# Kernel optimization log

Measured on AMD Instinct MI355X. Metric: run time of the kernel, lower is better.

The kernel has to match this reference:

```python
import jax, jax.numpy as jnp
import numpy as np

N_NODES = 100000
N_EDGES = 1600000
D_IN = 64
D_H = 64
D_LIN = 256
D_OUT = 128
N_GRAPHS = 64
BN_EPS = 1e-5


def setup_inputs() -> dict:
    key = jax.random.key(0)
    ks = jax.random.split(key, 16)

    def lin(k, fan_in, fan_out):
        # kaiming-ish init, scale 1/sqrt(fan_in)
        return jax.random.normal(k, (fan_in, fan_out), jnp.float32) / np.float32(np.sqrt(fan_in))

    inp = {}
    inp["x"] = jax.random.normal(ks[0], (N_NODES, D_IN), jnp.float32)
    inp["edge_index"] = jax.random.randint(ks[1], (2, N_EDGES), 0, N_NODES, jnp.int32)
    inp["batch"] = jnp.sort(jax.random.randint(ks[2], (N_NODES,), 0, N_GRAPHS, jnp.int32))

    dims = [(D_IN, D_H), (D_H, D_H), (D_H, D_H)]
    ki = 3
    for l, (di, do) in enumerate(dims):
        inp[f"conv{l}_w1"] = lin(ks[ki], di, do); ki += 1
        inp[f"conv{l}_b1"] = jnp.zeros((do,), jnp.float32)
        inp[f"conv{l}_w2"] = lin(ks[ki], do, do); ki += 1
        inp[f"conv{l}_b2"] = jnp.zeros((do,), jnp.float32)
    for l in range(2):
        inp[f"bn{l}_gamma"] = jnp.ones((D_H,), jnp.float32)
        inp[f"bn{l}_beta"] = jnp.zeros((D_H,), jnp.float32)
    inp["mp_w1"] = lin(ks[ki], D_H, D_LIN); ki += 1
    inp["mp_b1"] = jnp.zeros((D_LIN,), jnp.float32)
    inp["mp_w2"] = lin(ks[ki], D_LIN, D_OUT)
    inp["mp_b2"] = jnp.zeros((D_OUT,), jnp.float32)
    return inp


def gin_conv(x, src, dst, w1, b1, w2, b2):
    # GINConv with eps=0: nn((1+eps)*x + sum_{j->i} x_j)
    agg = jax.ops.segment_sum(x[src], dst, num_segments=N_NODES)  # [N, d]
    h = x + agg
    h = jnp.maximum(h @ w1 + b1, 0.0)
    return h @ w2 + b2


def batch_norm(x, gamma, beta):
    # BatchNorm1d over node dim (training-mode batch statistics)
    mean = jnp.mean(x, axis=0)
    var = jnp.var(x, axis=0)
    return (x - mean) * jax.lax.rsqrt(var + BN_EPS) * gamma + beta


def reference(x, edge_index, batch,
              conv0_w1, conv0_b1, conv0_w2, conv0_b2,
              conv1_w1, conv1_b1, conv1_w2, conv1_b2,
              conv2_w1, conv2_b1, conv2_w2, conv2_b2,
              bn0_gamma, bn0_beta, bn1_gamma, bn1_beta,
              mp_w1, mp_b1, mp_w2, mp_b2):
    src, dst = edge_index[0], edge_index[1]
    convs = [(conv0_w1, conv0_b1, conv0_w2, conv0_b2),
             (conv1_w1, conv1_b1, conv1_w2, conv1_b2),
             (conv2_w1, conv2_b1, conv2_w2, conv2_b2)]
    bns = [(bn0_gamma, bn0_beta), (bn1_gamma, bn1_beta)]

    h = x
    # first conv_num_layers-1 layers: conv -> BN -> ReLU (dropout = identity in eval)
    for i in range(2):
        w1, b1, w2, b2 = convs[i]
        h = gin_conv(h, src, dst, w1, b1, w2, b2)
        h = batch_norm(h, bns[i][0], bns[i][1])
        h = jnp.maximum(h, 0.0)
    # last conv
    w1, b1, w2, b2 = convs[2]
    h = gin_conv(h, src, dst, w1, b1, w2, b2)
    # global add pool over graphs
    pooled = jax.ops.segment_sum(h, batch, num_segments=N_GRAPHS)  # [G, d]
    emb = pooled
    out = jnp.maximum(pooled @ mp_w1 + mp_b1, 0.0)  # dropout = identity in eval
    out = out @ mp_w2 + mp_b2
    return (out, emb)
```

## Files before the change

kernel.cpp:

```cpp
#include <hip/hip_runtime.h>

#define N_NODES 100000
#define N_EDGES 1600000
#define D 64
#define N_GRAPHS 64
#define D_LIN 256
#define D_OUT 128
#define BN_EPS 1e-5f

typedef unsigned short ushort;
typedef unsigned int uint;

__device__ __forceinline__ float4 ld4(const float* p) { return *(const float4*)p; }

__device__ __forceinline__ uint f2bf(float f) {
  uint u = __float_as_uint(f);
  return (u + 0x7FFFu + ((u >> 16) & 1u)) >> 16;
}

__global__ __launch_bounds__(256) void k_cvt(const float* __restrict__ in,
                                             ushort* __restrict__ out, int n8) {
  int i = blockIdx.x * 256 + threadIdx.x;
  if (i < n8) {
    float4 a = ((const float4*)in)[2 * i];
    float4 b = ((const float4*)in)[2 * i + 1];
    uint4 o;
    o.x = f2bf(a.x) | (f2bf(a.y) << 16);
    o.y = f2bf(a.z) | (f2bf(a.w) << 16);
    o.z = f2bf(b.x) | (f2bf(b.y) << 16);
    o.w = f2bf(b.z) | (f2bf(b.w) << 16);
    ((uint4*)out)[i] = o;
  }
}

__global__ void k_count(const int* __restrict__ dstA, int* __restrict__ deg) {
  int i = blockIdx.x * blockDim.x + threadIdx.x;
  if (i < N_EDGES) atomicAdd(&deg[dstA[i]], 1);
}

__global__ void k_blocksum(const int* __restrict__ deg, int* __restrict__ bsum) {
  __shared__ int s[256];
  int t = threadIdx.x, i = blockIdx.x * 256 + t;
  s[t] = (i < N_NODES) ? deg[i] : 0;
  __syncthreads();
  for (int off = 128; off > 0; off >>= 1) {
    if (t < off) s[t] += s[t + off];
    __syncthreads();
  }
  if (t == 0) bsum[blockIdx.x] = s[0];
}

__global__ void k_scanblocks(const int* __restrict__ bsum, int* __restrict__ boff, int nb) {
  __shared__ int s[512];
  int t = threadIdx.x;
  int v = (t < nb) ? bsum[t] : 0;
  s[t] = v;
  __syncthreads();
  for (int off = 1; off < 512; off <<= 1) {
    int u = (t >= off) ? s[t - off] : 0;
    __syncthreads();
    s[t] += u;
    __syncthreads();
  }
  if (t < nb) boff[t] = s[t] - v;
}

__global__ void k_scanfinal(const int* __restrict__ deg, const int* __restrict__ boff,
                            int* __restrict__ rowptr, int* __restrict__ rowcur) {
  __shared__ int s[256];
  int t = threadIdx.x, i = blockIdx.x * 256 + t;
  int d = (i < N_NODES) ? deg[i] : 0;
  s[t] = d;
  __syncthreads();
  for (int off = 1; off < 256; off <<= 1) {
    int u = (t >= off) ? s[t - off] : 0;
    __syncthreads();
    s[t] += u;
    __syncthreads();
  }
  if (i < N_NODES) {
    int v = boff[blockIdx.x] + s[t] - d;
    rowptr[i] = v;
    rowcur[i] = v;
  }
  if (i == 0) rowptr[N_NODES] = N_EDGES;
}

__global__ void k_fill(const int* __restrict__ srcA, const int* __restrict__ dstA,
                       int* __restrict__ rowcur, int* __restrict__ colidx) {
  int i = blockIdx.x * blockDim.x + threadIdx.x;
  if (i < N_EDGES) {
    int d = dstA[i];
    int pos = atomicAdd(&rowcur[d], 1);
    colidx[pos] = srcA[i];
  }
}

template <int APPLY_BN, int EMIT_STATS, int OUT_BF>
__global__ __launch_bounds__(256, 6) void k_conv(
    const ushort* __restrict__ h_in, const float* __restrict__ ss,
    const int* __restrict__ rowptr, const int* __restrict__ colidx,
    const float* __restrict__ w1, const float* __restrict__ b1,
    const float* __restrict__ w2, const float* __restrict__ b2,
    float* __restrict__ h_out_f, ushort* __restrict__ h_out_bf,
    float* __restrict__ stats) {
  __shared__ float sT[64][68];
  __shared__ float sSum[64], sSq[64];

  const int tid = threadIdx.x;
  const int wave = tid >> 6, lane = tid & 63;
  const int eg = lane >> 3;
  const int fl = (lane & 7) << 3;
  const int row0 = blockIdx.x * 64;

  if (EMIT_STATS && tid < 64) { sSum[tid] = 0.f; sSq[tid] = 0.f; }

  float sc[8], sh[8];
  if (APPLY_BN) {
    float4 a = ld4(&ss[fl]), b = ld4(&ss[fl + 4]);
    float4 c = ld4(&ss[64 + fl]), d = ld4(&ss[64 + fl + 4]);
    sc[0] = a.x; sc[1] = a.y; sc[2] = a.z; sc[3] = a.w;
    sc[4] = b.x; sc[5] = b.y; sc[6] = b.z; sc[7] = b.w;
    sh[0] = c.x; sh[1] = c.y; sh[2] = c.z; sh[3] = c.w;
    sh[4] = d.x; sh[5] = d.y; sh[6] = d.z; sh[7] = d.w;
  }

#define ACC8(u)                                                        \
  {                                                                    \
    float f0 = __uint_as_float((u).x << 16);                           \
    float f1 = __uint_as_float((u).x & 0xffff0000u);                   \
    float f2 = __uint_as_float((u).y << 16);                           \
    float f3 = __uint_as_float((u).y & 0xffff0000u);                   \
    float f4 = __uint_as_float((u).z << 16);                           \
    float f5 = __uint_as_float((u).z & 0xffff0000u);                   \
    float f6 = __uint_as_float((u).w << 16);                           \
    float f7 = __uint_as_float((u).w & 0xffff0000u);                   \
    if (APPLY_BN) {                                                    \
      f0 = fmaxf(fmaf(f0, sc[0], sh[0]), 0.f);                         \
      f1 = fmaxf(fmaf(f1, sc[1], sh[1]), 0.f);                         \
      f2 = fmaxf(fmaf(f2, sc[2], sh[2]), 0.f);                         \
      f3 = fmaxf(fmaf(f3, sc[3], sh[3]), 0.f);                         \
      f4 = fmaxf(fmaf(f4, sc[4], sh[4]), 0.f);                         \
      f5 = fmaxf(fmaf(f5, sc[5], sh[5]), 0.f);                         \
      f6 = fmaxf(fmaf(f6, sc[6], sh[6]), 0.f);                         \
      f7 = fmaxf(fmaf(f7, sc[7], sh[7]), 0.f);                         \
    }                                                                  \
    acc[0] += f0; acc[1] += f1; acc[2] += f2; acc[3] += f3;            \
    acc[4] += f4; acc[5] += f5; acc[6] += f6; acc[7] += f7;            \
  }

  for (int rr = 0; rr < 16; ++rr) {
    const int r = (wave << 4) + rr;
    const int row = row0 + r;
    float acc[8] = {0.f, 0.f, 0.f, 0.f, 0.f, 0.f, 0.f, 0.f};
    if (row < N_NODES) {
      if (eg == 0) {
        uint4 u = *(const uint4*)(h_in + ((size_t)row << 6) + fl);
        ACC8(u);
      }
      const int e0 = rowptr[row], e1 = rowptr[row + 1];
      int e = e0 + eg;
      for (; e + 8 < e1; e += 16) {
        int s0 = colidx[e];
        int s1 = colidx[e + 8];
        uint4 u0 = *(const uint4*)(h_in + ((size_t)s0 << 6) + fl);
        uint4 u1 = *(const uint4*)(h_in + ((size_t)s1 << 6) + fl);
        ACC8(u0);
        ACC8(u1);
      }
      if (e < e1) {
        int s0 = colidx[e];
        uint4 u0 = *(const uint4*)(h_in + ((size_t)s0 << 6) + fl);
        ACC8(u0);
      }
#pragma unroll
      for (int j = 0; j < 8; ++j) {
        acc[j] += __shfl_xor(acc[j], 8);
        acc[j] += __shfl_xor(acc[j], 16);
        acc[j] += __shfl_xor(acc[j], 32);
      }
    }
    if (lane < 8) {
      *(float4*)&sT[r][fl] = make_float4(acc[0], acc[1], acc[2], acc[3]);
      *(float4*)&sT[r][fl + 4] = make_float4(acc[4], acc[5], acc[6], acc[7]);
    }
  }
#undef ACC8
  __syncthreads();

  const int tc = tid & 15, tr = tid >> 4;

  float hreg[4][4];
  {
    float acc[4][4];
#pragma unroll
    for (int i = 0; i < 4; ++i)
#pragma unroll
      for (int j = 0; j < 4; ++j) acc[i][j] = 0.f;
#pragma unroll 8
    for (int k = 0; k < 64; ++k) {
      const float4 b = ld4(&w1[(k << 6) + (tc << 2)]);
#pragma unroll
      for (int i = 0; i < 4; ++i) {
        const float a = sT[(tr << 2) + i][k];
        acc[i][0] = fmaf(a, b.x, acc[i][0]);
        acc[i][1] = fmaf(a, b.y, acc[i][1]);
        acc[i][2] = fmaf(a, b.z, acc[i][2]);
        acc[i][3] = fmaf(a, b.w, acc[i][3]);
      }
    }
    const float4 bb = ld4(&b1[tc << 2]);
#pragma unroll
    for (int i = 0; i < 4; ++i) {
      hreg[i][0] = fmaxf(acc[i][0] + bb.x, 0.f);
      hreg[i][1] = fmaxf(acc[i][1] + bb.y, 0.f);
      hreg[i][2] = fmaxf(acc[i][2] + bb.z, 0.f);
      hreg[i][3] = fmaxf(acc[i][3] + bb.w, 0.f);
    }
  }
  __syncthreads();
#pragma unroll
  for (int i = 0; i < 4; ++i)
    *(float4*)&sT[(tr << 2) + i][tc << 2] = *(float4*)&hreg[i][0];
  __syncthreads();

  {
    float acc[4][4];
#pragma unroll
    for (int i = 0; i < 4; ++i)
#pragma unroll
      for (int j = 0; j < 4; ++j) acc[i][j] = 0.f;
#pragma unroll 8
    for (int k = 0; k < 64; ++k) {
      const float4 b = ld4(&w2[(k << 6) + (tc << 2)]);
#pragma unroll
      for (int i = 0; i < 4; ++i) {
        const float a = sT[(tr << 2) + i][k];
        acc[i][0] = fmaf(a, b.x, acc[i][0]);
        acc[i][1] = fmaf(a, b.y, acc[i][1]);
        acc[i][2] = fmaf(a, b.z, acc[i][2]);
        acc[i][3] = fmaf(a, b.w, acc[i][3]);
      }
    }
    const float4 bb = ld4(&b2[tc << 2]);
    float p[4] = {0.f, 0.f, 0.f, 0.f}, q[4] = {0.f, 0.f, 0.f, 0.f};
#pragma unroll
    for (int i = 0; i < 4; ++i) {
      const int row = row0 + (tr << 2) + i;
      float4 o;
      o.x = acc[i][0] + bb.x;
      o.y = acc[i][1] + bb.y;
      o.z = acc[i][2] + bb.z;
      o.w = acc[i][3] + bb.w;
      if (row < N_NODES) {
        if (OUT_BF) {
          uint2 o2;
          o2.x = f2bf(o.x) | (f2bf(o.y) << 16);
          o2.y = f2bf(o.z) | (f2bf(o.w) << 16);
          *(uint2*)(h_out_bf + ((size_t)row << 6) + (tc << 2)) = o2;
        } else {
          *(float4*)&h_out_f[row * 64 + (tc << 2)] = o;
        }
        if (EMIT_STATS) {
          p[0] += o.x; q[0] += o.x * o.x;
          p[1] += o.y; q[1] += o.y * o.y;
          p[2] += o.z; q[2] += o.z * o.z;
          p[3] += o.w; q[3] += o.w * o.w;
        }
      }
    }
    if (EMIT_STATS) {
#pragma unroll
      for (int j = 0; j < 4; ++j) {
        atomicAdd(&sSum[(tc << 2) + j], p[j]);
        atomicAdd(&sSq[(tc << 2) + j], q[j]);
      }
      __syncthreads();
      if (tid < 64) {
        atomicAdd(&stats[tid], sSum[tid]);
        atomicAdd(&stats[64 + tid], sSq[tid]);
      }
    }
  }
}

__global__ void k_bnfin(const float* __restrict__ stats, const float* __restrict__ gamma,
                        const float* __restrict__ beta, float* __restrict__ ss) {
  int t = threadIdx.x;
  if (t < 64) {
    const float inv_n = 1.f / (float)N_NODES;
    float mean = stats[t] * inv_n;
    float var = stats[64 + t] * inv_n - mean * mean;
    float scale = gamma[t] * rsqrtf(var + BN_EPS);
    ss[t] = scale;
    ss[64 + t] = beta[t] - mean * scale;
  }
}

__global__ __launch_bounds__(256) void k_pool(const float* __restrict__ h,
                                              const int* __restrict__ batch,
                                              float* __restrict__ emb) {
  const int NW = 1024;
  const int RPW = (N_NODES + NW - 1) / NW;
  int wid = (blockIdx.x * 256 + threadIdx.x) >> 6;
  int lane = threadIdx.x & 63;
  int r0 = wid * RPW;
  if (r0 >= N_NODES) return;
  int r1 = min(r0 + RPW, N_NODES);
  float acc = 0.f;
  int curg = batch[r0];
  for (int i = r0; i < r1; ++i) {
    int g = batch[i];
    if (g != curg) {
      atomicAdd(&emb[curg * 64 + lane], acc);
      acc = 0.f;
      curg = g;
    }
    acc += h[i * 64 + lane];
  }
  atomicAdd(&emb[curg * 64 + lane], acc);
}

__global__ __launch_bounds__(256) void k_mlp(const float* __restrict__ emb,
                                             const float* __restrict__ w1,
                                             const float* __restrict__ b1,
                                             const float* __restrict__ w2,
                                             const float* __restrict__ b2,
                                             float* __restrict__ out) {
  __shared__ float sp[64];
  __shared__ float smid[256];
  int g = blockIdx.x, t = threadIdx.x;
  if (t < 64) sp[t] = emb[g * 64 + t];
  __syncthreads();
  float acc = b1[t];
#pragma unroll 8
  for (int k = 0; k < 64; ++k) acc = fmaf(sp[k], w1[k * 256 + t], acc);
  smid[t] = fmaxf(acc, 0.f);
  __syncthreads();
  if (t < 128) {
    float o = b2[t];
#pragma unroll 8
    for (int k = 0; k < 256; ++k) o = fmaf(smid[k], w2[k * 128 + t], o);
    out[g * 128 + t] = o;
  }
}

extern "C" void kernel_launch(void* const* d_in, const int* in_sizes, int n_in,
                              void* d_out, int out_size, void* d_ws, size_t ws_size,
                              hipStream_t stream) {
  const float* x = (const float*)d_in[0];
  const int* edge = (const int*)d_in[1];
  const int* batch = (const int*)d_in[2];
  const float* cw1[3] = {(const float*)d_in[3], (const float*)d_in[7], (const float*)d_in[11]};
  const float* cb1[3] = {(const float*)d_in[4], (const float*)d_in[8], (const float*)d_in[12]};
  const float* cw2[3] = {(const float*)d_in[5], (const float*)d_in[9], (const float*)d_in[13]};
  const float* cb2[3] = {(const float*)d_in[6], (const float*)d_in[10], (const float*)d_in[14]};
  const float* bng[2] = {(const float*)d_in[15], (const float*)d_in[17]};
  const float* bnb[2] = {(const float*)d_in[16], (const float*)d_in[18]};
  const float* mpw1 = (const float*)d_in[19];
  const float* mpb1 = (const float*)d_in[20];
  const float* mpw2 = (const float*)d_in[21];
  const float* mpb2 = (const float*)d_in[22];

  char* ws = (char*)d_ws;
  size_t off = 0;
  auto alloc = [&](size_t bytes) {
    void* p = ws + off;
    off = (off + bytes + 255) & ~(size_t)255;
    return p;
  };
  int* rowptr = (int*)alloc((N_NODES + 1) * sizeof(int));
  int* rowcur = (int*)alloc(N_NODES * sizeof(int));
  int* colidx = (int*)alloc(N_EDGES * sizeof(int));
  int* bsum = (int*)alloc(512 * sizeof(int));
  int* boff = (int*)alloc(512 * sizeof(int));
  ushort* x_bf = (ushort*)alloc((size_t)N_NODES * 64 * sizeof(ushort));
  ushort* hA_bf = (ushort*)alloc((size_t)N_NODES * 64 * sizeof(ushort));
  ushort* hB_bf = (ushort*)alloc((size_t)N_NODES * 64 * sizeof(ushort));
  float* stats = (float*)alloc(2 * 128 * sizeof(float));
  float* ssbuf = (float*)alloc(2 * 128 * sizeof(float));
  float* hF = (float*)x_bf;

  float* outp = (float*)d_out;
  float* emb = outp + N_GRAPHS * D_OUT;

  const int* srcA = edge;
  const int* dstA = edge + N_EDGES;

  hipMemsetAsync(rowcur, 0, N_NODES * sizeof(int), stream);
  hipMemsetAsync(stats, 0, 2 * 128 * sizeof(float), stream);
  hipMemsetAsync(emb, 0, N_GRAPHS * 64 * sizeof(float), stream);

  const int NB = (N_NODES + 255) / 256;
  const int EB = (N_EDGES + 255) / 256;
  k_cvt<<<(N_NODES * 64 / 8 + 255) / 256, 256, 0, stream>>>(x, x_bf, N_NODES * 64 / 8);
  k_count<<<EB, 256, 0, stream>>>(dstA, rowcur);
  k_blocksum<<<NB, 256, 0, stream>>>(rowcur, bsum);
  k_scanblocks<<<1, 512, 0, stream>>>(bsum, boff, NB);
  k_scanfinal<<<NB, 256, 0, stream>>>(rowcur, boff, rowptr, rowcur);
  k_fill<<<EB, 256, 0, stream>>>(srcA, dstA, rowcur, colidx);

  const int GC = (N_NODES + 63) / 64;
  k_conv<0, 1, 1><<<GC, 256, 0, stream>>>(x_bf, nullptr, rowptr, colidx, cw1[0], cb1[0],
                                          cw2[0], cb2[0], nullptr, hA_bf, stats);
  k_bnfin<<<1, 64, 0, stream>>>(stats, bng[0], bnb[0], ssbuf);
  k_conv<1, 1, 1><<<GC, 256, 0, stream>>>(hA_bf, ssbuf, rowptr, colidx, cw1[1], cb1[1],
                                          cw2[1], cb2[1], nullptr, hB_bf, stats + 128);
  k_bnfin<<<1, 64, 0, stream>>>(stats + 128, bng[1], bnb[1], ssbuf + 128);
  k_conv<1, 0, 0><<<GC, 256, 0, stream>>>(hB_bf, ssbuf + 128, rowptr, colidx, cw1[2],
                                          cb1[2], cw2[2], cb2[2], hF, nullptr, nullptr);

  k_pool<<<256, 256, 0, stream>>>(hF, batch, emb);
  k_mlp<<<N_GRAPHS, 256, 0, stream>>>(emb, mpw1, mpb1, mpw2, mpb2, outp);
}
```

Before: 537.9 us.

## Build CSR via bucketed two-pass binning and shrink conv blocks to 32 rows

Result: no change. 534.0 us (-0.7%).

```diff
diff --git a/kernel.cpp b/kernel.cpp
--- a/kernel.cpp
+++ b/kernel.cpp
@@ -7,6 +7,8 @@
 #define D_LIN 256
 #define D_OUT 128
 #define BN_EPS 1e-5f
+#define NBUCK 782
+#define BIN_CH 16384
 
 typedef unsigned short ushort;
 typedef unsigned int uint;
@@ -33,85 +35,132 @@
   }
 }
 
-__global__ void k_count(const int* __restrict__ dstA, int* __restrict__ deg) {
-  int i = blockIdx.x * blockDim.x + threadIdx.x;
-  if (i < N_EDGES) atomicAdd(&deg[dstA[i]], 1);
-}
-
-__global__ void k_blocksum(const int* __restrict__ deg, int* __restrict__ bsum) {
-  __shared__ int s[256];
-  int t = threadIdx.x, i = blockIdx.x * 256 + t;
-  s[t] = (i < N_NODES) ? deg[i] : 0;
-  __syncthreads();
-  for (int off = 128; off > 0; off >>= 1) {
-    if (t < off) s[t] += s[t + off];
-    __syncthreads();
-  }
-  if (t == 0) bsum[blockIdx.x] = s[0];
-}
-
-__global__ void k_scanblocks(const int* __restrict__ bsum, int* __restrict__ boff, int nb) {
-  __shared__ int s[512];
+
+__global__ __launch_bounds__(256) void k_hist(const int* __restrict__ dstA,
+                                              int* __restrict__ bcnt) {
+  __shared__ int lh[NBUCK];
+  for (int i = threadIdx.x; i < NBUCK; i += 256) lh[i] = 0;
+  __syncthreads();
+  int i = blockIdx.x * 256 + threadIdx.x;
+  const int stride = gridDim.x * 256;
+  for (; i < N_EDGES; i += stride) atomicAdd(&lh[dstA[i] >> 7], 1);
+  __syncthreads();
+  for (int i = threadIdx.x; i < NBUCK; i += 256)
+    if (lh[i]) atomicAdd(&bcnt[i], lh[i]);
+}
+
+__global__ __launch_bounds__(1024) void k_bscan(const int* __restrict__ bcnt,
+                                                int* __restrict__ boff,
+                                                int* __restrict__ bcur) {
+  __shared__ int s[1024];
   int t = threadIdx.x;
-  int v = (t < nb) ? bsum[t] : 0;
+  int v = (t < NBUCK) ? bcnt[t] : 0;
   s[t] = v;
   __syncthreads();
-  for (int off = 1; off < 512; off <<= 1) {
+  for (int off = 1; off < 1024; off <<= 1) {
     int u = (t >= off) ? s[t - off] : 0;
     __syncthreads();
     s[t] += u;
     __syncthreads();
   }
-  if (t < nb) boff[t] = s[t] - v;
-}
-
-__global__ void k_scanfinal(const int* __restrict__ deg, const int* __restrict__ boff,
-                            int* __restrict__ rowptr, int* __restrict__ rowcur) {
-  __shared__ int s[256];
-  int t = threadIdx.x, i = blockIdx.x * 256 + t;
-  int d = (i < N_NODES) ? deg[i] : 0;
-  s[t] = d;
-  __syncthreads();
-  for (int off = 1; off < 256; off <<= 1) {
-    int u = (t >= off) ? s[t - off] : 0;
+  if (t < NBUCK) {
+    boff[t] = s[t] - v;
+    bcur[t] = s[t] - v;
+  }
+}
+
+__global__ __launch_bounds__(256) void k_bin(const int* __restrict__ srcA,
+                                             const int* __restrict__ dstA,
+                                             int* __restrict__ bcur,
+                                             uint2* __restrict__ pairs) {
+  __shared__ int lh[NBUCK];
+  __shared__ int lbase[NBUCK];
+  const int tid = threadIdx.x;
+  for (int i = tid; i < NBUCK; i += 256) lh[i] = 0;
+  __syncthreads();
+  const int e0 = blockIdx.x * BIN_CH;
+  const int e1 = min(e0 + BIN_CH, N_EDGES);
+  for (int i = e0 + tid; i < e1; i += 256) atomicAdd(&lh[dstA[i] >> 7], 1);
+  __syncthreads();
+  for (int b = tid; b < NBUCK; b += 256) {
+    int c = lh[b];
+    if (c) lbase[b] = atomicAdd(&bcur[b], c);
+  }
+  __syncthreads();
+  for (int b = tid; b < NBUCK; b += 256) lh[b] = 0;
+  __syncthreads();
+  for (int i = e0 + tid; i < e1; i += 256) {
+    int d = dstA[i];
+    int b = d >> 7;
+    int p = lbase[b] + atomicAdd(&lh[b], 1);
+    pairs[p] = make_uint2((uint)srcA[i], (uint)d);
+  }
+}
+
+__global__ __launch_bounds__(256) void k_bucket(const uint2* __restrict__ pairs,
+                                                const int* __restrict__ boff,
+                                                const int* __restrict__ bcnt,
+                                                int* __restrict__ rowptr,
+                                                int* __restrict__ colidx) {
+  __shared__ int ldeg[128], lsc[128], lcur[128];
+  __shared__ int stage[4096];
+  const int tid = threadIdx.x;
+  const int b = blockIdx.x;
+  const int node0 = b << 7;
+  const int base = boff[b], cnt = bcnt[b];
+  if (tid < 128) ldeg[tid] = 0;
+  __syncthreads();
+  for (int i = tid; i < cnt; i += 256) atomicAdd(&ldeg[pairs[base + i].y & 127], 1);
+  __syncthreads();
+  if (tid < 128) lsc[tid] = ldeg[tid];
+  __syncthreads();
+  for (int off = 1; off < 128; off <<= 1) {
+    int u = (tid < 128 && tid >= off) ? lsc[tid - off] : 0;
     __syncthreads();
-    s[t] += u;
+    if (tid < 128) lsc[tid] += u;
     __syncthreads();
   }
-  if (i < N_NODES) {
-    int v = boff[blockIdx.x] + s[t] - d;
-    rowptr[i] = v;
-    rowcur[i] = v;
-  }
-  if (i == 0) rowptr[N_NODES] = N_EDGES;
-}
-
-__global__ void k_fill(const int* __restrict__ srcA, const int* __restrict__ dstA,
-                       int* __restrict__ rowcur, int* __restrict__ colidx) {
-  int i = blockIdx.x * blockDim.x + threadIdx.x;
-  if (i < N_EDGES) {
-    int d = dstA[i];
-    int pos = atomicAdd(&rowcur[d], 1);
-    colidx[pos] = srcA[i];
+  if (tid < 128) {
+    int excl = lsc[tid] - ldeg[tid];
+    lcur[tid] = excl;
+    int node = node0 + tid;
+    if (node < N_NODES) rowptr[node] = base + excl;
+  }
+  if (b == NBUCK - 1 && tid == 0) rowptr[N_NODES] = N_EDGES;
+  __syncthreads();
+  if (cnt <= 4096) {
+    for (int i = tid; i < cnt; i += 256) {
+      uint2 pr = pairs[base + i];
+      int p = atomicAdd(&lcur[pr.y & 127], 1);
+      stage[p] = (int)pr.x;
+    }
+    __syncthreads();
+    for (int i = tid; i < cnt; i += 256) colidx[base + i] = stage[i];
+  } else {
+    for (int i = tid; i < cnt; i += 256) {
+      uint2 pr = pairs[base + i];
+      int p = atomicAdd(&lcur[pr.y & 127], 1);
+      colidx[base + p] = (int)pr.x;
+    }
   }
 }
 
 template <int APPLY_BN, int EMIT_STATS, int OUT_BF>
-__global__ __launch_bounds__(256, 6) void k_conv(
+__global__ __launch_bounds__(128, 8) void k_conv(
     const ushort* __restrict__ h_in, const float* __restrict__ ss,
     const int* __restrict__ rowptr, const int* __restrict__ colidx,
     const float* __restrict__ w1, const float* __restrict__ b1,
     const float* __restrict__ w2, const float* __restrict__ b2,
     float* __restrict__ h_out_f, ushort* __restrict__ h_out_bf,
     float* __restrict__ stats) {
-  __shared__ float sT[64][68];
+  __shared__ float sT[32][68];
   __shared__ float sSum[64], sSq[64];
 
   const int tid = threadIdx.x;
   const int wave = tid >> 6, lane = tid & 63;
   const int eg = lane >> 3;
   const int fl = (lane & 7) << 3;
-  const int row0 = blockIdx.x * 64;
+  const int row0 = blockIdx.x * 32;
 
   if (EMIT_STATS && tid < 64) { sSum[tid] = 0.f; sSq[tid] = 0.f; }
 
@@ -153,32 +202,30 @@
     const int r = (wave << 4) + rr;
     const int row = row0 + r;
     float acc[8] = {0.f, 0.f, 0.f, 0.f, 0.f, 0.f, 0.f, 0.f};
-    if (row < N_NODES) {
-      if (eg == 0) {
-        uint4 u = *(const uint4*)(h_in + ((size_t)row << 6) + fl);
-        ACC8(u);
-      }
-      const int e0 = rowptr[row], e1 = rowptr[row + 1];
-      int e = e0 + eg;
-      for (; e + 8 < e1; e += 16) {
-        int s0 = colidx[e];
-        int s1 = colidx[e + 8];
-        uint4 u0 = *(const uint4*)(h_in + ((size_t)s0 << 6) + fl);
-        uint4 u1 = *(const uint4*)(h_in + ((size_t)s1 << 6) + fl);
-        ACC8(u0);
-        ACC8(u1);
-      }
-      if (e < e1) {
-        int s0 = colidx[e];
-        uint4 u0 = *(const uint4*)(h_in + ((size_t)s0 << 6) + fl);
-        ACC8(u0);
-      }
-#pragma unroll
-      for (int j = 0; j < 8; ++j) {
-        acc[j] += __shfl_xor(acc[j], 8);
-        acc[j] += __shfl_xor(acc[j], 16);
-        acc[j] += __shfl_xor(acc[j], 32);
-      }
+    if (eg == 0) {
+      uint4 u = *(const uint4*)(h_in + ((size_t)row << 6) + fl);
+      ACC8(u);
+    }
+    const int e0 = rowptr[row], e1 = rowptr[row + 1];
+    int e = e0 + eg;
+    for (; e + 8 < e1; e += 16) {
+      int s0 = colidx[e];
+      int s1 = colidx[e + 8];
+      uint4 u0 = *(const uint4*)(h_in + ((size_t)s0 << 6) + fl);
+      uint4 u1 = *(const uint4*)(h_in + ((size_t)s1 << 6) + fl);
+      ACC8(u0);
+      ACC8(u1);
+    }
+    if (e < e1) {
+      int s0 = colidx[e];
+      uint4 u0 = *(const uint4*)(h_in + ((size_t)s0 << 6) + fl);
+      ACC8(u0);
+    }
+#pragma unroll
+    for (int j = 0; j < 8; ++j) {
+      acc[j] += __shfl_xor(acc[j], 8);
+      acc[j] += __shfl_xor(acc[j], 16);
+      acc[j] += __shfl_xor(acc[j], 32);
     }
     if (lane < 8) {
       *(float4*)&sT[r][fl] = make_float4(acc[0], acc[1], acc[2], acc[3]);
@@ -252,21 +299,19 @@
       o.y = acc[i][1] + bb.y;
       o.z = acc[i][2] + bb.z;
       o.w = acc[i][3] + bb.w;
-      if (row < N_NODES) {
-        if (OUT_BF) {
-          uint2 o2;
-          o2.x = f2bf(o.x) | (f2bf(o.y) << 16);
-          o2.y = f2bf(o.z) | (f2bf(o.w) << 16);
-          *(uint2*)(h_out_bf + ((size_t)row << 6) + (tc << 2)) = o2;
-        } else {
-          *(float4*)&h_out_f[row * 64 + (tc << 2)] = o;
-        }
-        if (EMIT_STATS) {
-          p[0] += o.x; q[0] += o.x * o.x;
-          p[1] += o.y; q[1] += o.y * o.y;
-          p[2] += o.z; q[2] += o.z * o.z;
-          p[3] += o.w; q[3] += o.w * o.w;
-        }
+      if (OUT_BF) {
+        uint2 o2;
+        o2.x = f2bf(o.x) | (f2bf(o.y) << 16);
+        o2.y = f2bf(o.z) | (f2bf(o.w) << 16);
+        *(uint2*)(h_out_bf + ((size_t)row << 6) + (tc << 2)) = o2;
+      } else {
+        *(float4*)&h_out_f[row * 64 + (tc << 2)] = o;
+      }
+      if (EMIT_STATS) {
+        p[0] += o.x; q[0] += o.x * o.x;
+        p[1] += o.y; q[1] += o.y * o.y;
+        p[2] += o.z; q[2] += o.z * o.z;
+        p[3] += o.w; q[3] += o.w * o.w;
       }
     }
     if (EMIT_STATS) {
@@ -370,16 +415,17 @@
     return p;
   };
   int* rowptr = (int*)alloc((N_NODES + 1) * sizeof(int));
-  int* rowcur = (int*)alloc(N_NODES * sizeof(int));
   int* colidx = (int*)alloc(N_EDGES * sizeof(int));
-  int* bsum = (int*)alloc(512 * sizeof(int));
-  int* boff = (int*)alloc(512 * sizeof(int));
+  int* bcnt = (int*)alloc(NBUCK * sizeof(int));
+  int* boff = (int*)alloc(NBUCK * sizeof(int));
+  int* bcur = (int*)alloc(NBUCK * sizeof(int));
   ushort* x_bf = (ushort*)alloc((size_t)N_NODES * 64 * sizeof(ushort));
   ushort* hA_bf = (ushort*)alloc((size_t)N_NODES * 64 * sizeof(ushort));
   ushort* hB_bf = (ushort*)alloc((size_t)N_NODES * 64 * sizeof(ushort));
   float* stats = (float*)alloc(2 * 128 * sizeof(float));
   float* ssbuf = (float*)alloc(2 * 128 * sizeof(float));
   float* hF = (float*)x_bf;
+  uint2* pairs = (uint2*)hB_bf;
 
   float* outp = (float*)d_out;
   float* emb = outp + N_GRAPHS * D_OUT;
@@ -387,27 +433,24 @@
   const int* srcA = edge;
   const int* dstA = edge + N_EDGES;
 
-  hipMemsetAsync(rowcur, 0, N_NODES * sizeof(int), stream);
+  hipMemsetAsync(bcnt, 0, NBUCK * sizeof(int), stream);
   hipMemsetAsync(stats, 0, 2 * 128 * sizeof(float), stream);
   hipMemsetAsync(emb, 0, N_GRAPHS * 64 * sizeof(float), stream);
 
-  const int NB = (N_NODES + 255) / 256;
-  const int EB = (N_EDGES + 255) / 256;
   k_cvt<<<(N_NODES * 64 / 8 + 255) / 256, 256, 0, stream>>>(x, x_bf, N_NODES * 64 / 8);
-  k_count<<<EB, 256, 0, stream>>>(dstA, rowcur);
-  k_blocksum<<<NB, 256, 0, stream>>>(rowcur, bsum);
-  k_scanblocks<<<1, 512, 0, stream>>>(bsum, boff, NB);
-  k_scanfinal<<<NB, 256, 0, stream>>>(rowcur, boff, rowptr, rowcur);
-  k_fill<<<EB, 256, 0, stream>>>(srcA, dstA, rowcur, colidx);
-
-  const int GC = (N_NODES + 63) / 64;
-  k_conv<0, 1, 1><<<GC, 256, 0, stream>>>(x_bf, nullptr, rowptr, colidx, cw1[0], cb1[0],
+  k_hist<<<256, 256, 0, stream>>>(dstA, bcnt);
+  k_bscan<<<1, 1024, 0, stream>>>(bcnt, boff, bcur);
+  k_bin<<<(N_EDGES + BIN_CH - 1) / BIN_CH, 256, 0, stream>>>(srcA, dstA, bcur, pairs);
+  k_bucket<<<NBUCK, 256, 0, stream>>>(pairs, boff, bcnt, rowptr, colidx);
+
+  const int GC = N_NODES / 32;
+  k_conv<0, 1, 1><<<GC, 128, 0, stream>>>(x_bf, nullptr, rowptr, colidx, cw1[0], cb1[0],
                                           cw2[0], cb2[0], nullptr, hA_bf, stats);
   k_bnfin<<<1, 64, 0, stream>>>(stats, bng[0], bnb[0], ssbuf);
-  k_conv<1, 1, 1><<<GC, 256, 0, stream>>>(hA_bf, ssbuf, rowptr, colidx, cw1[1], cb1[1],
+  k_conv<1, 1, 1><<<GC, 128, 0, stream>>>(hA_bf, ssbuf, rowptr, colidx, cw1[1], cb1[1],
                                           cw2[1], cb2[1], nullptr, hB_bf, stats + 128);
   k_bnfin<<<1, 64, 0, stream>>>(stats + 128, bng[1], bnb[1], ssbuf + 128);
-  k_conv<1, 0, 0><<<GC, 256, 0, stream>>>(hB_bf, ssbuf + 128, rowptr, colidx, cw1[2],
+  k_conv<1, 0, 0><<<GC, 128, 0, stream>>>(hB_bf, ssbuf + 128, rowptr, colidx, cw1[2],
                                           cb1[2], cw2[2], cb2[2], hF, nullptr, nullptr);
 
   k_pool<<<256, 256, 0, stream>>>(hF, batch, emb);
```
